# Kernel optimization log

Measured on AMD Instinct MI355X. Metric: run time of the kernel, lower is better.

The kernel has to match this reference:

```python
import jax, jax.numpy as jnp
import numpy as np

NB_HEAD = 16
SIZE_PER_HEAD = 64
D_MODEL = NB_HEAD * SIZE_PER_HEAD  # 1024
B, L = 2, 2048
NEG_BIG = 1e12


def setup_inputs() -> dict:
    key = jax.random.key(0)
    ks = jax.random.split(key, 8)
    return {
        "Q_seq": jax.random.normal(ks[0], (B, L, D_MODEL), dtype=jnp.float32),
        "K_seq": jax.random.normal(ks[1], (B, L, D_MODEL), dtype=jnp.float32),
        "V_seq": jax.random.normal(ks[2], (B, L, D_MODEL), dtype=jnp.float32),
        "q_len": jax.random.randint(ks[3], (B, 1), 1, L, dtype=jnp.int32),
        "v_len": jax.random.randint(ks[4], (B, 1), 1, L, dtype=jnp.int32),
        "WQ": jax.random.normal(ks[5], (D_MODEL, D_MODEL), dtype=jnp.float32) * 0.02,
        "WK": jax.random.normal(ks[6], (D_MODEL, D_MODEL), dtype=jnp.float32) * 0.02,
        "WV": jax.random.normal(ks[7], (D_MODEL, D_MODEL), dtype=jnp.float32) * 0.02,
    }


def _len_mask(lens, length, dtype):
    # Keras code: mask = 1 - cumsum(one_hot(len, L)) -> 1 for pos < len, 0 otherwise
    return (jnp.arange(length)[None, :] < lens).astype(dtype)  # [B, L]


def reference(Q_seq, K_seq, V_seq, q_len, v_len, WQ, WK, WV):
    Bq, Lq, _ = Q_seq.shape
    Lk = K_seq.shape[1]
    # QKV projections, split heads: [B, H, L, D]
    q = (Q_seq @ WQ).reshape(Bq, Lq, NB_HEAD, SIZE_PER_HEAD).transpose(0, 2, 1, 3)
    k = (K_seq @ WK).reshape(Bq, Lk, NB_HEAD, SIZE_PER_HEAD).transpose(0, 2, 1, 3)
    v = (V_seq @ WV).reshape(Bq, Lk, NB_HEAD, SIZE_PER_HEAD).transpose(0, 2, 1, 3)
    # scaled dot-product scores [B, H, Lq, Lk]
    scores = jnp.einsum("bhqd,bhkd->bhqk", q, k) / np.float32(SIZE_PER_HEAD ** 0.5)
    # additive key-length mask (V_len), matching Mask(..., 'add')
    kmask = _len_mask(v_len, Lk, scores.dtype)  # [B, Lk]
    scores = scores - (1.0 - kmask)[:, None, None, :] * np.float32(NEG_BIG)
    A = jax.nn.softmax(scores, axis=-1)
    # attention output, merge heads: [B, Lq, H*D]
    O = jnp.einsum("bhqk,bhkd->bqhd", A, v).reshape(Bq, Lq, D_MODEL)
    # multiplicative query-length mask (Q_len), matching Mask(..., 'mul')
    qmask = _len_mask(q_len, Lq, O.dtype)  # [B, Lq]
    return O * qmask[:, :, None]
```

## Files before the change

kernel.cpp:

```cpp
#include <hip/hip_runtime.h>
#include <cstddef>

#define NB_HEAD 16
#define HEAD_DIM 64
#define D_MODEL 1024
#define BATCH 2
#define SEQ 2048
#define MROWS (BATCH * SEQ)

typedef __bf16 bf16x8 __attribute__((ext_vector_type(8)));
typedef __bf16 bf16x4 __attribute__((ext_vector_type(4)));
typedef float  f32x4  __attribute__((ext_vector_type(4)));

#define XEL ((size_t)MROWS * D_MODEL)
#define WEL ((size_t)D_MODEL * D_MODEL)

static __device__ __forceinline__ size_t xchunk(int row, int k) {
    return ((size_t)(row >> 4) * 32 + (k >> 5)) * 512 + ((k >> 3) & 3) * 128 + (row & 15) * 8 + (k & 7);
}
static __device__ __forceinline__ size_t qkbase(int bh, int row16, int dc) {
    return ((size_t)(bh * 128 + row16) * 2 + dc) * 512;
}
static __device__ __forceinline__ size_t qkelem(int bh, int row, int d) {
    return qkbase(bh, row >> 4, d >> 5) + ((d >> 3) & 3) * 128 + (row & 15) * 8 + (d & 7);
}
static __device__ __forceinline__ size_t vbase(int bh, int d16, int kc) {
    return ((size_t)(bh * 4 + d16) * 64 + kc) * 512;
}
static __device__ __forceinline__ size_t velem(int bh, int d, int key) {
    return vbase(bh, d >> 4, key >> 5) + ((key >> 3) & 3) * 128 + (d & 15) * 8 + (key & 7);
}

static __device__ __forceinline__ void split_bf16(float x, __bf16& h, __bf16& l) {
    h = (__bf16)x;
    l = (__bf16)(x - (float)h);
}

__global__ __launch_bounds__(256) void conv_wt_kernel(
    const float* __restrict__ W0, const float* __restrict__ W1,
    const float* __restrict__ W2,
    __bf16* __restrict__ hi, __bf16* __restrict__ lo)
{
    __shared__ float tile[64][65];
    const int t  = threadIdx.x;
    const int k0 = blockIdx.x * 64;
    const int n0 = blockIdx.y * 64;
    const int z  = blockIdx.z;
    const float* W = (z == 0) ? W0 : ((z == 1) ? W1 : W2);
    __bf16* hz = hi + (size_t)z * WEL;
    __bf16* lz = lo + (size_t)z * WEL;

    #pragma unroll
    for (int p = 0; p < 4; ++p) {
        const int e = (p * 256 + t) * 4;
        const int r = e >> 6, c = e & 63;
        const float4 v = *(const float4*)(W + (size_t)(k0 + r) * D_MODEL + n0 + c);
        tile[r][c] = v.x; tile[r][c + 1] = v.y; tile[r][c + 2] = v.z; tile[r][c + 3] = v.w;
    }
    __syncthreads();
    #pragma unroll
    for (int p = 0; p < 4; ++p) {
        const int e = (p * 256 + t) * 4;
        const int n = e >> 6, kc = e & 63;
        __bf16 h[4], l[4];
        #pragma unroll
        for (int u = 0; u < 4; ++u) split_bf16(tile[kc + u][n], h[u], l[u]);
        const size_t a = xchunk(n0 + n, k0 + kc);
        *(bf16x4*)(hz + a) = (bf16x4){h[0], h[1], h[2], h[3]};
        *(bf16x4*)(lz + a) = (bf16x4){l[0], l[1], l[2], l[3]};
    }
}

__global__ __launch_bounds__(256) void conv_x_kernel(
    const float* __restrict__ X0, const float* __restrict__ X1,
    const float* __restrict__ X2,
    const int* __restrict__ q_len, const int* __restrict__ v_len,
    __bf16* __restrict__ xhi, __bf16* __restrict__ xlo)
{
    const int z = blockIdx.y;
    const size_t e = ((size_t)blockIdx.x * 256 + threadIdx.x) * 8;
    const int l = (int)(e >> 10);
    const int bb = l >> 11, lb = l & (SEQ - 1);
    const int len = (z == 0) ? q_len[bb] : v_len[bb];
    if (lb >= ((len + 127) & ~127)) return;

    const float* X = (z == 0) ? X0 : ((z == 1) ? X1 : X2);
    const float4 v0 = *(const float4*)(X + e);
    const float4 v1 = *(const float4*)(X + e + 4);
    const float xs[8] = {v0.x, v0.y, v0.z, v0.w, v1.x, v1.y, v1.z, v1.w};
    bf16x8 h8, l8;
    #pragma unroll
    for (int u = 0; u < 8; ++u) { __bf16 h_, l_; split_bf16(xs[u], h_, l_); h8[u] = h_; l8[u] = l_; }
    const size_t a = z * XEL + xchunk(l, (int)(e & 1023));
    *(bf16x8*)(xhi + a) = h8;
    *(bf16x8*)(xlo + a) = l8;
}

__global__ __launch_bounds__(256, 3) void proj_mfma_kernel(
    const __bf16* __restrict__ Xhi, const __bf16* __restrict__ Xlo,
    const __bf16* __restrict__ Wchi, const __bf16* __restrict__ Wclo,
    const int* __restrict__ q_len, const int* __restrict__ v_len,
    __bf16* __restrict__ qch, __bf16* __restrict__ qcl,
    __bf16* __restrict__ kch, __bf16* __restrict__ kcl,
    __bf16* __restrict__ vch, __bf16* __restrict__ vcl)
{
    const int t    = threadIdx.x;
    const int wave = t >> 6, lane = t & 63;
    const int li   = lane & 15, grp = lane >> 4;
    const int wm   = wave >> 1, wn = wave & 1;
    const int m0   = blockIdx.x * 64;
    const int n0   = blockIdx.y * 128;
    const int z    = blockIdx.z;
    const int bb   = m0 >> 11;
    const int l0   = m0 & (SEQ - 1);
    const int need = (z == 0) ? q_len[bb] : v_len[bb];
    if (l0 >= need) return;

    const __bf16* Xh = Xhi + z * XEL;
    const __bf16* Xl = Xlo + z * XEL;
    const __bf16* Wh = Wchi + z * WEL;
    const __bf16* Wl = Wclo + z * WEL;

    const size_t abase = ((size_t)((m0 >> 4) + wm * 2) * 32) * 512 + lane * 8;
    const size_t bbase = ((size_t)((n0 >> 4) + wn * 4) * 32) * 512 + lane * 8;

    f32x4 acc[2][4] = {};
    bf16x8 ah[2][2], al[2][2], bh[2][4], bl[2][4];

    #pragma unroll
    for (int i = 0; i < 2; ++i) {
        ah[0][i] = *(const bf16x8*)(Xh + abase + (size_t)i * 16384);
        al[0][i] = *(const bf16x8*)(Xl + abase + (size_t)i * 16384);
    }
    #pragma unroll
    for (int j = 0; j < 4; ++j) {
        bh[0][j] = *(const bf16x8*)(Wh + bbase + (size_t)j * 16384);
        bl[0][j] = *(const bf16x8*)(Wl + bbase + (size_t)j * 16384);
    }

    #pragma unroll 2
    for (int kc = 0; kc < 32; ++kc) {
        const int cur = kc & 1, nxt = cur ^ 1;
        if (kc < 31) {
            const size_t ka = abase + (size_t)(kc + 1) * 512;
            const size_t kb = bbase + (size_t)(kc + 1) * 512;
            #pragma unroll
            for (int i = 0; i < 2; ++i) {
                ah[nxt][i] = *(const bf16x8*)(Xh + ka + (size_t)i * 16384);
                al[nxt][i] = *(const bf16x8*)(Xl + ka + (size_t)i * 16384);
            }
            #pragma unroll
            for (int j = 0; j < 4; ++j) {
                bh[nxt][j] = *(const bf16x8*)(Wh + kb + (size_t)j * 16384);
                bl[nxt][j] = *(const bf16x8*)(Wl + kb + (size_t)j * 16384);
            }
        }
        #pragma unroll
        for (int j = 0; j < 4; ++j)
            #pragma unroll
            for (int i = 0; i < 2; ++i) {
                acc[i][j] = __builtin_amdgcn_mfma_f32_16x16x32_bf16(ah[cur][i], bh[cur][j], acc[i][j], 0, 0, 0);
                acc[i][j] = __builtin_amdgcn_mfma_f32_16x16x32_bf16(ah[cur][i], bl[cur][j], acc[i][j], 0, 0, 0);
                acc[i][j] = __builtin_amdgcn_mfma_f32_16x16x32_bf16(al[cur][i], bh[cur][j], acc[i][j], 0, 0, 0);
            }
    }

    const float oscale = (z == 0) ? 0.125f : 1.0f;
    #pragma unroll
    for (int j = 0; j < 4; ++j) {
        const int cg = n0 + wn * 64 + j * 16 + li;
        const int hd = cg >> 6, d = cg & 63;
        const int bhI = bb * NB_HEAD + hd;
        #pragma unroll
        for (int i = 0; i < 2; ++i) {
            #pragma unroll
            for (int r = 0; r < 4; ++r) {
                const int rg = m0 + wm * 32 + i * 16 + grp * 4 + r;
                const int lg = rg & (SEQ - 1);
                __bf16 h_, l_;
                split_bf16(acc[i][j][r] * oscale, h_, l_);
                if (z == 0) {
                    const size_t a = qkelem(bhI, lg, d);
                    qch[a] = h_; qcl[a] = l_;
                } else if (z == 1) {
                    const size_t a = qkelem(bhI, lg, d);
                    kch[a] = h_; kcl[a] = l_;
                } else {
                    const size_t a = velem(bhI, d, lg);
                    vch[a] = h_; vcl[a] = l_;
                }
            }
        }
    }
}

__global__ __launch_bounds__(256, 2) void attn_mfma_kernel(
    const __bf16* __restrict__ qch, const __bf16* __restrict__ qcl,
    const __bf16* __restrict__ kch, const __bf16* __restrict__ kcl,
    const __bf16* __restrict__ vch, const __bf16* __restrict__ vcl,
    const int* __restrict__ q_len, const int* __restrict__ v_len,
    float* __restrict__ out)
{
    __shared__ __align__(16) __bf16 Ps[128][132];

    const int t = threadIdx.x;
    const int wq = t >> 6, lane = t & 63;
    const int grp = lane >> 4, li = lane & 15;
    const int hh = blockIdx.x;
    const int q0 = blockIdx.y * 128;
    const int b  = blockIdx.z;
    const int qlen = q_len[b], vlen = v_len[b];
    const int bh = b * NB_HEAD + hh;
    const int qbase = q0 + wq * 32;

    if (qbase >= qlen) {
        const int row = qbase + (lane >> 1), cs = (lane & 1) * 32;
        float* o = out + ((size_t)b * SEQ + row) * D_MODEL + hh * HEAD_DIM + cs;
        const float4 z4 = make_float4(0.f, 0.f, 0.f, 0.f);
        #pragma unroll
        for (int u = 0; u < 8; ++u) *(float4*)(o + u * 4) = z4;
        return;
    }

    bf16x8 qh[2][2], ql[2][2];
    #pragma unroll
    for (int s = 0; s < 2; ++s)
        #pragma unroll
        for (int ks = 0; ks < 2; ++ks) {
            const size_t a = qkbase(bh, (qbase >> 4) + s, ks) + lane * 8;
            qh[s][ks] = *(const bf16x8*)(qch + a);
            ql[s][ks] = *(const bf16x8*)(qcl + a);
        }

    f32x4 O[2][4] = {};
    float m_s[2][4], l_s[2][4];
    #pragma unroll
    for (int s = 0; s < 2; ++s)
        #pragma unroll
        for (int r = 0; r < 4; ++r) { m_s[s][r] = -1e30f; l_s[s][r] = 0.f; }

    const int nkt = (vlen + 127) >> 7;

    for (int tt = 0; tt < nkt; ++tt) {
        const int k0 = tt * 128;
        const bool full = (k0 + 128 <= vlen);

        f32x4 sacc[2][8] = {};
        #pragma unroll
        for (int ks = 0; ks < 2; ++ks) {
            #pragma unroll
            for (int j = 0; j < 8; ++j) {
                const size_t a = qkbase(bh, (k0 >> 4) + j, ks) + lane * 8;
                const bf16x8 kh_ = *(const bf16x8*)(kch + a);
                const bf16x8 kl_ = *(const bf16x8*)(kcl + a);
                #pragma unroll
                for (int s = 0; s < 2; ++s) {
                    sacc[s][j] = __builtin_amdgcn_mfma_f32_16x16x32_bf16(qh[s][ks], kh_, sacc[s][j], 0, 0, 0);
                    sacc[s][j] = __builtin_amdgcn_mfma_f32_16x16x32_bf16(qh[s][ks], kl_, sacc[s][j], 0, 0, 0);
                    sacc[s][j] = __builtin_amdgcn_mfma_f32_16x16x32_bf16(ql[s][ks], kh_, sacc[s][j], 0, 0, 0);
                }
            }
        }

        #pragma unroll
        for (int s = 0; s < 2; ++s) {
            float mx[4] = {-1e30f, -1e30f, -1e30f, -1e30f};
            if (!full) {
                #pragma unroll
                for (int j = 0; j < 8; ++j) {
                    const int key = k0 + j * 16 + li;
                    #pragma unroll
                    for (int r = 0; r < 4; ++r) {
                        float v = sacc[s][j][r];
                        if (key >= vlen) v = -1e30f;
                        sacc[s][j][r] = v;
                        mx[r] = fmaxf(mx[r], v);
                    }
                }
            } else {
                #pragma unroll
                for (int j = 0; j < 8; ++j)
                    #pragma unroll
                    for (int r = 0; r < 4; ++r) mx[r] = fmaxf(mx[r], sacc[s][j][r]);
            }
            #pragma unroll
            for (int r = 0; r < 4; ++r) {
                mx[r] = fmaxf(mx[r], __shfl_xor(mx[r], 1));
                mx[r] = fmaxf(mx[r], __shfl_xor(mx[r], 2));
                mx[r] = fmaxf(mx[r], __shfl_xor(mx[r], 4));
                mx[r] = fmaxf(mx[r], __shfl_xor(mx[r], 8));
            }
            float al[4], sum[4];
            #pragma unroll
            for (int r = 0; r < 4; ++r) {
                const float mn = fmaxf(m_s[s][r], mx[r]);
                al[r] = __expf(m_s[s][r] - mn);
                m_s[s][r] = mn;
                sum[r] = 0.f;
            }
            #pragma unroll
            for (int j = 0; j < 8; ++j)
                #pragma unroll
                for (int r = 0; r < 4; ++r) {
                    const float p = __expf(sacc[s][j][r] - m_s[s][r]);
                    const __bf16 pb = (__bf16)p;
                    sum[r] += (float)pb;
                    Ps[wq * 32 + s * 16 + grp * 4 + r][j * 16 + li] = pb;
                }
            #pragma unroll
            for (int r = 0; r < 4; ++r) {
                sum[r] += __shfl_xor(sum[r], 1);
                sum[r] += __shfl_xor(sum[r], 2);
                sum[r] += __shfl_xor(sum[r], 4);
                sum[r] += __shfl_xor(sum[r], 8);
                l_s[s][r] = l_s[s][r] * al[r] + sum[r];
            }
            #pragma unroll
            for (int j = 0; j < 4; ++j)
                #pragma unroll
                for (int r = 0; r < 4; ++r) O[s][j][r] *= al[r];
        }

        #pragma unroll
        for (int ks = 0; ks < 4; ++ks) {
            bf16x8 pa[2];
            #pragma unroll
            for (int s = 0; s < 2; ++s)
                pa[s] = *(const bf16x8*)&Ps[wq * 32 + s * 16 + li][ks * 32 + grp * 8];
            #pragma unroll
            for (int j = 0; j < 4; ++j) {
                const size_t a = vbase(bh, j, (k0 >> 5) + ks) + lane * 8;
                const bf16x8 vh_ = *(const bf16x8*)(vch + a);
                const bf16x8 vl_ = *(const bf16x8*)(vcl + a);
                #pragma unroll
                for (int s = 0; s < 2; ++s) {
                    O[s][j] = __builtin_amdgcn_mfma_f32_16x16x32_bf16(pa[s], vh_, O[s][j], 0, 0, 0);
                    O[s][j] = __builtin_amdgcn_mfma_f32_16x16x32_bf16(pa[s], vl_, O[s][j], 0, 0, 0);
                }
            }
        }
    }

    #pragma unroll
    for (int s = 0; s < 2; ++s)
        #pragma unroll
        for (int r = 0; r < 4; ++r) {
            const int q = qbase + s * 16 + grp * 4 + r;
            const float inv = (q < qlen) ? 1.f / l_s[s][r] : 0.f;
            #pragma unroll
            for (int j = 0; j < 4; ++j)
                out[((size_t)b * SEQ + q) * D_MODEL + hh * HEAD_DIM + j * 16 + li] = O[s][j][r] * inv;
        }
}

extern "C" void kernel_launch(void* const* d_in, const int* in_sizes, int n_in,
                              void* d_out, int out_size, void* d_ws, size_t ws_size,
                              hipStream_t stream)
{
    (void)in_sizes; (void)n_in; (void)out_size; (void)ws_size;
    const float* Q_seq = (const float*)d_in[0];
    const float* K_seq = (const float*)d_in[1];
    const float* V_seq = (const float*)d_in[2];
    const int*   q_len = (const int*)d_in[3];
    const int*   v_len = (const int*)d_in[4];
    const float* WQ    = (const float*)d_in[5];
    const float* WK    = (const float*)d_in[6];
    const float* WV    = (const float*)d_in[7];
    float* out = (float*)d_out;

    __bf16* wchi = (__bf16*)d_ws;
    __bf16* wclo = wchi + 3 * WEL;
    __bf16* xhi_ = wclo + 3 * WEL;
    __bf16* xlo_ = xhi_ + 3 * XEL;
    __bf16* qch_ = xlo_ + 3 * XEL;
    __bf16* qcl_ = qch_ + XEL;
    __bf16* kch_ = qcl_ + XEL;
    __bf16* kcl_ = kch_ + XEL;
    __bf16* vch_ = kcl_ + XEL;
    __bf16* vcl_ = vch_ + XEL;

    dim3 blk(256);

    dim3 cg(D_MODEL / 64, D_MODEL / 64, 3);
    conv_wt_kernel<<<cg, blk, 0, stream>>>(WQ, WK, WV, wchi, wclo);

    dim3 xg((unsigned)(XEL / 2048), 3);
    conv_x_kernel<<<xg, blk, 0, stream>>>(Q_seq, K_seq, V_seq, q_len, v_len, xhi_, xlo_);

    dim3 pg(MROWS / 64, D_MODEL / 128, 3);
    proj_mfma_kernel<<<pg, blk, 0, stream>>>(xhi_, xlo_, wchi, wclo, q_len, v_len,
                                             qch_, qcl_, kch_, kcl_, vch_, vcl_);

    dim3 ag(NB_HEAD, SEQ / 128, BATCH);
    attn_mfma_kernel<<<ag, blk, 0, stream>>>(qch_, qcl_, kch_, kcl_, vch_, vcl_,
                                             q_len, v_len, out);
}
```

Measured before the change: 308.9 us.

## Split K-reduction across wave pairs in projection and attention kernels

The projection kernel now gives each pair of waves the same 64x64 output tile and splits the K dimension between them. Partial sums are combined through shared memory, and V is written with vectorized bf16x4 stores. The attention kernel halves the query tile to 64 rows per block and splits the key tiles between two waves, merging their softmax state (max and sum) and outputs in shared memory; V fragments are also prefetched ahead of the PV MFMAs. This doubles the number of attention blocks and gives each wave more independent work, at the cost of extra shared-memory reduction, higher register pressure and changed launch bounds.

```diff
diff --git a/kernel.cpp b/kernel.cpp
--- a/kernel.cpp
+++ b/kernel.cpp
@@ -96,7 +96,7 @@
     *(bf16x8*)(xlo + a) = l8;
 }
 
-__global__ __launch_bounds__(256, 3) void proj_mfma_kernel(
+__global__ __launch_bounds__(256, 2) void proj_mfma_kernel(
     const __bf16* __restrict__ Xhi, const __bf16* __restrict__ Xlo,
     const __bf16* __restrict__ Wchi, const __bf16* __restrict__ Wclo,
     const int* __restrict__ q_len, const int* __restrict__ v_len,
@@ -104,10 +104,12 @@
     __bf16* __restrict__ kch, __bf16* __restrict__ kcl,
     __bf16* __restrict__ vch, __bf16* __restrict__ vcl)
 {
+    __shared__ __align__(16) float OB[2][4096];
+
     const int t    = threadIdx.x;
     const int wave = t >> 6, lane = t & 63;
     const int li   = lane & 15, grp = lane >> 4;
-    const int wm   = wave >> 1, wn = wave & 1;
+    const int wn   = wave >> 1, par = wave & 1;
     const int m0   = blockIdx.x * 64;
     const int n0   = blockIdx.y * 128;
     const int z    = blockIdx.z;
@@ -121,80 +123,105 @@
     const __bf16* Wh = Wchi + z * WEL;
     const __bf16* Wl = Wclo + z * WEL;
 
-    const size_t abase = ((size_t)((m0 >> 4) + wm * 2) * 32) * 512 + lane * 8;
+    const size_t abase = ((size_t)(m0 >> 4) * 32) * 512 + lane * 8;
     const size_t bbase = ((size_t)((n0 >> 4) + wn * 4) * 32) * 512 + lane * 8;
 
-    f32x4 acc[2][4] = {};
-    bf16x8 ah[2][2], al[2][2], bh[2][4], bl[2][4];
-
-    #pragma unroll
-    for (int i = 0; i < 2; ++i) {
-        ah[0][i] = *(const bf16x8*)(Xh + abase + (size_t)i * 16384);
-        al[0][i] = *(const bf16x8*)(Xl + abase + (size_t)i * 16384);
-    }
-    #pragma unroll
-    for (int j = 0; j < 4; ++j) {
-        bh[0][j] = *(const bf16x8*)(Wh + bbase + (size_t)j * 16384);
-        bl[0][j] = *(const bf16x8*)(Wl + bbase + (size_t)j * 16384);
+    f32x4 acc[4][4] = {};
+    bf16x8 ah[2][4], al[2][4], bh[2][4], bl[2][4];
+
+    #pragma unroll
+    for (int i = 0; i < 4; ++i) {
+        const size_t ka = abase + (size_t)par * 512 + (size_t)i * 16384;
+        const size_t kb = bbase + (size_t)par * 512 + (size_t)i * 16384;
+        ah[0][i] = *(const bf16x8*)(Xh + ka);
+        al[0][i] = *(const bf16x8*)(Xl + ka);
+        bh[0][i] = *(const bf16x8*)(Wh + kb);
+        bl[0][i] = *(const bf16x8*)(Wl + kb);
     }
 
     #pragma unroll 2
-    for (int kc = 0; kc < 32; ++kc) {
-        const int cur = kc & 1, nxt = cur ^ 1;
-        if (kc < 31) {
-            const size_t ka = abase + (size_t)(kc + 1) * 512;
-            const size_t kb = bbase + (size_t)(kc + 1) * 512;
-            #pragma unroll
-            for (int i = 0; i < 2; ++i) {
-                ah[nxt][i] = *(const bf16x8*)(Xh + ka + (size_t)i * 16384);
-                al[nxt][i] = *(const bf16x8*)(Xl + ka + (size_t)i * 16384);
-            }
-            #pragma unroll
-            for (int j = 0; j < 4; ++j) {
-                bh[nxt][j] = *(const bf16x8*)(Wh + kb + (size_t)j * 16384);
-                bl[nxt][j] = *(const bf16x8*)(Wl + kb + (size_t)j * 16384);
+    for (int it = 0; it < 16; ++it) {
+        const int cur = it & 1, nxt = cur ^ 1;
+        if (it < 15) {
+            const size_t koff = (size_t)(par + 2 * (it + 1)) * 512;
+            #pragma unroll
+            for (int i = 0; i < 4; ++i) {
+                const size_t ka = abase + koff + (size_t)i * 16384;
+                const size_t kb = bbase + koff + (size_t)i * 16384;
+                ah[nxt][i] = *(const bf16x8*)(Xh + ka);
+                al[nxt][i] = *(const bf16x8*)(Xl + ka);
+                bh[nxt][i] = *(const bf16x8*)(Wh + kb);
+                bl[nxt][i] = *(const bf16x8*)(Wl + kb);
             }
         }
         #pragma unroll
         for (int j = 0; j < 4; ++j)
             #pragma unroll
-            for (int i = 0; i < 2; ++i) {
+            for (int i = 0; i < 4; ++i) {
                 acc[i][j] = __builtin_amdgcn_mfma_f32_16x16x32_bf16(ah[cur][i], bh[cur][j], acc[i][j], 0, 0, 0);
                 acc[i][j] = __builtin_amdgcn_mfma_f32_16x16x32_bf16(ah[cur][i], bl[cur][j], acc[i][j], 0, 0, 0);
                 acc[i][j] = __builtin_amdgcn_mfma_f32_16x16x32_bf16(al[cur][i], bh[cur][j], acc[i][j], 0, 0, 0);
             }
     }
 
-    const float oscale = (z == 0) ? 0.125f : 1.0f;
-    #pragma unroll
-    for (int j = 0; j < 4; ++j) {
-        const int cg = n0 + wn * 64 + j * 16 + li;
-        const int hd = cg >> 6, d = cg & 63;
-        const int bhI = bb * NB_HEAD + hd;
-        #pragma unroll
-        for (int i = 0; i < 2; ++i) {
-            #pragma unroll
-            for (int r = 0; r < 4; ++r) {
-                const int rg = m0 + wm * 32 + i * 16 + grp * 4 + r;
-                const int lg = rg & (SEQ - 1);
-                __bf16 h_, l_;
-                split_bf16(acc[i][j][r] * oscale, h_, l_);
-                if (z == 0) {
-                    const size_t a = qkelem(bhI, lg, d);
-                    qch[a] = h_; qcl[a] = l_;
-                } else if (z == 1) {
-                    const size_t a = qkelem(bhI, lg, d);
-                    kch[a] = h_; kcl[a] = l_;
+    __syncthreads();
+    if (par == 1) {
+        #pragma unroll
+        for (int i = 0; i < 4; ++i)
+            #pragma unroll
+            for (int j = 0; j < 4; ++j)
+                #pragma unroll
+                for (int r = 0; r < 4; ++r)
+                    OB[wn][((i * 4 + j) * 4 + r) * 64 + lane] = acc[i][j][r];
+    }
+    __syncthreads();
+    if (par == 0) {
+        #pragma unroll
+        for (int i = 0; i < 4; ++i)
+            #pragma unroll
+            for (int j = 0; j < 4; ++j)
+                #pragma unroll
+                for (int r = 0; r < 4; ++r)
+                    acc[i][j][r] += OB[wn][((i * 4 + j) * 4 + r) * 64 + lane];
+
+        const float oscale = (z == 0) ? 0.125f : 1.0f;
+        #pragma unroll
+        for (int j = 0; j < 4; ++j) {
+            const int cg = n0 + wn * 64 + j * 16 + li;
+            const int hd = cg >> 6, d = cg & 63;
+            const int bhI = bb * NB_HEAD + hd;
+            #pragma unroll
+            for (int i = 0; i < 4; ++i) {
+                if (z < 2) {
+                    #pragma unroll
+                    for (int r = 0; r < 4; ++r) {
+                        const int rg = m0 + i * 16 + grp * 4 + r;
+                        const int lg = rg & (SEQ - 1);
+                        __bf16 h_, l_;
+                        split_bf16(acc[i][j][r] * oscale, h_, l_);
+                        const size_t a = qkelem(bhI, lg, d);
+                        if (z == 0) { qch[a] = h_; qcl[a] = l_; }
+                        else        { kch[a] = h_; kcl[a] = l_; }
+                    }
                 } else {
-                    const size_t a = velem(bhI, d, lg);
-                    vch[a] = h_; vcl[a] = l_;
-                }
-            }
-        }
-    }
-}
-
-__global__ __launch_bounds__(256, 2) void attn_mfma_kernel(
+                    const int lbase = l0 + i * 16 + grp * 4;
+                    bf16x4 ph, pl;
+                    #pragma unroll
+                    for (int r = 0; r < 4; ++r) {
+                        __bf16 h_, l_;
+                        split_bf16(acc[i][j][r], h_, l_);
+                        ph[r] = h_; pl[r] = l_;
+                    }
+                    const size_t a = velem(bhI, d, lbase);
+                    *(bf16x4*)(vch + a) = ph;
+                    *(bf16x4*)(vcl + a) = pl;
+                }
+            }
+        }
+    }
+}
+
+__global__ __launch_bounds__(256, 3) void attn_mfma_kernel(
     const __bf16* __restrict__ qch, const __bf16* __restrict__ qcl,
     const __bf16* __restrict__ kch, const __bf16* __restrict__ kcl,
     const __bf16* __restrict__ vch, const __bf16* __restrict__ vcl,
@@ -202,23 +229,26 @@
     float* __restrict__ out)
 {
     __shared__ __align__(16) __bf16 Ps[128][132];
+    __shared__ __align__(16) float OBuf[2][2048];
+    __shared__ float MB[2][32], LB[2][32];
 
     const int t = threadIdx.x;
     const int wq = t >> 6, lane = t & 63;
+    const int pair = wq >> 1, par = wq & 1;
     const int grp = lane >> 4, li = lane & 15;
     const int hh = blockIdx.x;
-    const int q0 = blockIdx.y * 128;
+    const int q0 = blockIdx.y * 64;
     const int b  = blockIdx.z;
     const int qlen = q_len[b], vlen = v_len[b];
     const int bh = b * NB_HEAD + hh;
-    const int qbase = q0 + wq * 32;
-
-    if (qbase >= qlen) {
-        const int row = qbase + (lane >> 1), cs = (lane & 1) * 32;
+    const int qbase = q0 + pair * 32;
+
+    if (q0 >= qlen) {
+        const int row = q0 + (t >> 2), cs = (t & 3) * 16;
         float* o = out + ((size_t)b * SEQ + row) * D_MODEL + hh * HEAD_DIM + cs;
         const float4 z4 = make_float4(0.f, 0.f, 0.f, 0.f);
         #pragma unroll
-        for (int u = 0; u < 8; ++u) *(float4*)(o + u * 4) = z4;
+        for (int u = 0; u < 4; ++u) *(float4*)(o + u * 4) = z4;
         return;
     }
 
@@ -239,9 +269,9 @@
         #pragma unroll
         for (int r = 0; r < 4; ++r) { m_s[s][r] = -1e30f; l_s[s][r] = 0.f; }
 
-    const int nkt = (vlen + 127) >> 7;
-
-    for (int tt = 0; tt < nkt; ++tt) {
+    const int nkt_w = (qbase < qlen) ? ((vlen + 127) >> 7) : 0;
+
+    for (int tt = par; tt < nkt_w; tt += 2) {
         const int k0 = tt * 128;
         const bool full = (k0 + 128 <= vlen);
 
@@ -261,6 +291,16 @@
                 }
             }
         }
+
+        bf16x8 vh_[4][4], vl_[4][4];
+        #pragma unroll
+        for (int ks = 0; ks < 4; ++ks)
+            #pragma unroll
+            for (int j = 0; j < 4; ++j) {
+                const size_t a = vbase(bh, j, (k0 >> 5) + ks) + lane * 8;
+                vh_[ks][j] = *(const bf16x8*)(vch + a);
+                vl_[ks][j] = *(const bf16x8*)(vcl + a);
+            }
 
         #pragma unroll
         for (int s = 0; s < 2; ++s) {
@@ -328,29 +368,57 @@
             for (int s = 0; s < 2; ++s)
                 pa[s] = *(const bf16x8*)&Ps[wq * 32 + s * 16 + li][ks * 32 + grp * 8];
             #pragma unroll
-            for (int j = 0; j < 4; ++j) {
-                const size_t a = vbase(bh, j, (k0 >> 5) + ks) + lane * 8;
-                const bf16x8 vh_ = *(const bf16x8*)(vch + a);
-                const bf16x8 vl_ = *(const bf16x8*)(vcl + a);
+            for (int j = 0; j < 4; ++j)
                 #pragma unroll
                 for (int s = 0; s < 2; ++s) {
-                    O[s][j] = __builtin_amdgcn_mfma_f32_16x16x32_bf16(pa[s], vh_, O[s][j], 0, 0, 0);
-                    O[s][j] = __builtin_amdgcn_mfma_f32_16x16x32_bf16(pa[s], vl_, O[s][j], 0, 0, 0);
-                }
-            }
-        }
-    }
-
-    #pragma unroll
-    for (int s = 0; s < 2; ++s)
-        #pragma unroll
-        for (int r = 0; r < 4; ++r) {
-            const int q = qbase + s * 16 + grp * 4 + r;
-            const float inv = (q < qlen) ? 1.f / l_s[s][r] : 0.f;
+                    O[s][j] = __builtin_amdgcn_mfma_f32_16x16x32_bf16(pa[s], vh_[ks][j], O[s][j], 0, 0, 0);
+                    O[s][j] = __builtin_amdgcn_mfma_f32_16x16x32_bf16(pa[s], vl_[ks][j], O[s][j], 0, 0, 0);
+                }
+        }
+    }
+
+    __syncthreads();
+    if (par == 1) {
+        #pragma unroll
+        for (int s = 0; s < 2; ++s)
             #pragma unroll
             for (int j = 0; j < 4; ++j)
-                out[((size_t)b * SEQ + q) * D_MODEL + hh * HEAD_DIM + j * 16 + li] = O[s][j][r] * inv;
-        }
+                #pragma unroll
+                for (int r = 0; r < 4; ++r)
+                    OBuf[pair][((s * 4 + j) * 4 + r) * 64 + lane] = O[s][j][r];
+        if (li == 0) {
+            #pragma unroll
+            for (int s = 0; s < 2; ++s)
+                #pragma unroll
+                for (int r = 0; r < 4; ++r) {
+                    const int row = s * 16 + grp * 4 + r;
+                    MB[pair][row] = m_s[s][r];
+                    LB[pair][row] = l_s[s][r];
+                }
+        }
+    }
+    __syncthreads();
+    if (par == 0) {
+        #pragma unroll
+        for (int s = 0; s < 2; ++s)
+            #pragma unroll
+            for (int r = 0; r < 4; ++r) {
+                const int row = s * 16 + grp * 4 + r;
+                const int q = qbase + row;
+                const float m0_ = m_s[s][r], m1_ = MB[pair][row];
+                const float ms = fmaxf(m0_, m1_);
+                const float a0 = __expf(m0_ - ms), a1 = __expf(m1_ - ms);
+                const float lsum = l_s[s][r] * a0 + LB[pair][row] * a1;
+                const float inv = (q < qlen) ? 1.f / lsum : 0.f;
+                const float f0 = a0 * inv, f1 = a1 * inv;
+                #pragma unroll
+                for (int j = 0; j < 4; ++j) {
+                    const float o1 = OBuf[pair][((s * 4 + j) * 4 + r) * 64 + lane];
+                    out[((size_t)b * SEQ + q) * D_MODEL + hh * HEAD_DIM + j * 16 + li]
+                        = O[s][j][r] * f0 + o1 * f1;
+                }
+            }
+    }
 }
 
 extern "C" void kernel_launch(void* const* d_in, const int* in_sizes, int n_in,
@@ -391,7 +459,7 @@
     proj_mfma_kernel<<<pg, blk, 0, stream>>>(xhi_, xlo_, wchi, wclo, q_len, v_len,
                                              qch_, qcl_, kch_, kcl_, vch_, vcl_);
 
-    dim3 ag(NB_HEAD, SEQ / 128, BATCH);
+    dim3 ag(NB_HEAD, SEQ / 64, BATCH);
     attn_mfma_kernel<<<ag, blk, 0, stream>>>(qch_, qcl_, kch_, kcl_, vch_, vcl_,
                                              q_len, v_len, out);
 }
```

Result: slower. 430.5 us (+39.4%).
